# Kernel tuning notes

Hardware: AMD Instinct MI355X
Metric: run time of the kernel (lower is better)

The kernel has to match this reference:

```python
import jax, jax.numpy as jnp
import numpy as np

EPS = 1e-6


def _min_max_norm(v):
    # torch: 2.0 + (v - v.min()) / (v.max() - v.min()), global scalars
    mn, mx = v.min(), v.max()
    return 2.0 + (v - mn) / (mx - mn)


def setup_inputs() -> dict:
    key = jax.random.key(0)
    k1, k2, k3 = jax.random.split(key, 3)
    B, C, H, W = 2, 32, 96, 128
    return {
        "queries": jax.random.normal(k1, (B, C, H, W), jnp.float32),
        "keys": jax.random.normal(k2, (B, C, H, W), jnp.float32),
        "values": jax.random.normal(k3, (B, C, H, W), jnp.float32),
    }


def reference(queries, keys, values):
    B, C, H, W = queries.shape

    def row_column_softmax(s):  # s: [B,C,H,W]
        rc = jax.nn.softmax(s, axis=3) + jax.nn.softmax(s, axis=2)
        return rc / rc.max()

    def per_channel(q_c):  # q_c: [B,H,W] -> one output channel
        q = jnp.broadcast_to(q_c[:, None], (B, C, H, W))  # repeat over C
        # q_k_transpose: [B,C,H,H] (einsum sums w and y independently)
        hxh = jnp.einsum('bchw,bcxy->bchx', q, keys) + EPS
        # q_transpose_k: [B,C,W,W]
        wxw = jnp.einsum('bchw,bcxy->bcwy', q, keys) + EPS
        h_row = _min_max_norm(hxh.sum(axis=2))  # [B,C,H]  ('bcij->bcj')
        h_col = _min_max_norm(hxh.sum(axis=3))  # [B,C,H]  ('bcij->bci')
        w_row = _min_max_norm(wxw.sum(axis=2))  # [B,C,W]
        w_col = _min_max_norm(wxw.sum(axis=3))  # [B,C,W]
        outer = lambda m, n: jnp.einsum('bch,bcw->bchw', m, n)
        score = (row_column_softmax(outer(h_row, w_row))
                 + row_column_softmax(outer(h_row, w_col))
                 + row_column_softmax(outer(h_col, w_row))
                 + row_column_softmax(outer(h_col, w_col)))
        score = score / score.max()
        z_c = jnp.einsum('bchw,bchw->bhw', score, values)  # [B,H,W]
        return z_c, score

    # vectorize the original Python loop over query channels
    z_all, scores = jax.vmap(per_channel)(jnp.moveaxis(queries, 1, 0))
    z = jnp.swapaxes(z_all, 0, 1)  # [B,C,H,W]
    # torch returns the atten_score of the LAST loop iteration
    return z, scores[-1]
```

## Files before the change

kernel.cpp:

```cpp
#include <hip/hip_runtime.h>
#include <float.h>

#define BB 2
#define CC 32
#define HH 96
#define WW 128
#define HW (HH*WW)
#define BC (BB*CC)
#define NPLANE (BC*HW)
#define EPSF 1e-6f
#define LOG2E 1.4426950408889634f

#define QR_OFF 0
#define QC_OFF (QR_OFF + BC*HH)
#define QS_OFF (QC_OFF + BC*WW)
#define KR_OFF (QS_OFF + BC)
#define KC_OFF (KR_OFF + BC*HH)
#define KS_OFF (KC_OFF + BC*WW)
#define REC_OFF (KS_OFF + BC)
#define RECSZ 1344
#define BMX_OFF (REC_OFF + CC*BC*RECSZ)
#define BSX_OFF (BMX_OFF + CC*BC*4)

__device__ __forceinline__ float rcpf(float x) { return __builtin_amdgcn_rcpf(x); }
__device__ __forceinline__ float e2(float x) { return __builtin_amdgcn_exp2f(x); }

__device__ __forceinline__ float blkmax4(float v) {
  __shared__ float sred[4];
  #pragma unroll
  for (int o = 32; o > 0; o >>= 1) v = fmaxf(v, __shfl_xor(v, o, 64));
  if ((threadIdx.x & 63) == 0) sred[threadIdx.x >> 6] = v;
  __syncthreads();
  float r = fmaxf(fmaxf(sred[0], sred[1]), fmaxf(sred[2], sred[3]));
  __syncthreads();
  return r;
}

__global__ __launch_bounds__(256) void k1_plane_sums(const float* __restrict__ q,
                                                     const float* __restrict__ k,
                                                     float* __restrict__ ws) {
  int pb = blockIdx.x;
  int plane = pb & (BC - 1);
  const float* src = (pb < BC ? q : k) + (size_t)plane * HW;
  float* rowO = ws + (pb < BC ? QR_OFF : KR_OFF) + plane * HH;
  float* colO = ws + (pb < BC ? QC_OFF : KC_OFF) + plane * WW;
  float* totO = ws + (pb < BC ? QS_OFF : KS_OFF) + plane;
  __shared__ float cp[4 * WW];
  __shared__ float rsh[HH];
  __shared__ float wtot[2];
  int tid = threadIdx.x;
  int u = tid >> 6, l = tid & 63;
  float csum0 = 0.f, csum1 = 0.f;
  #pragma unroll 4
  for (int r = 0; r < 24; ++r) {
    int h = u * 24 + r;
    float v0 = src[h * WW + l];
    float v1 = src[h * WW + l + 64];
    csum0 += v0; csum1 += v1;
    float rs = v0 + v1;
    #pragma unroll
    for (int o = 1; o < 64; o <<= 1) rs += __shfl_xor(rs, o, 64);
    if (l == 0) { rowO[h] = rs; rsh[h] = rs; }
  }
  cp[u * WW + l] = csum0;
  cp[u * WW + l + 64] = csum1;
  __syncthreads();
  if (tid < WW) colO[tid] = cp[tid] + cp[WW + tid] + cp[2 * WW + tid] + cp[3 * WW + tid];
  float tv = (tid < HH) ? rsh[tid] : 0.f;
  if (tid < 128) {
    #pragma unroll
    for (int o = 1; o < 64; o <<= 1) tv += __shfl_xor(tv, o, 64);
    if ((tid & 63) == 0) wtot[tid >> 6] = tv;
  }
  __syncthreads();
  if (tid == 0) *totO = wtot[0] + wtot[1];
}

__device__ __forceinline__ float k2_raw(const float* __restrict__ ws, int type, int c0, int i, int L) {
  int bc = i / L, x = i - bc * L;
  int b = bc >> 5;
  if (type == 0) return ws[QS_OFF + b * CC + c0] * ws[KR_OFF + bc * HH + x] + HH * EPSF;
  if (type == 1) return ws[QR_OFF + (b * CC + c0) * HH + x] * ws[KS_OFF + bc] + HH * EPSF;
  if (type == 2) return ws[QS_OFF + b * CC + c0] * ws[KC_OFF + bc * WW + x] + WW * EPSF;
  return ws[QC_OFF + (b * CC + c0) * WW + x] * ws[KS_OFF + bc] + WW * EPSF;
}

__global__ __launch_bounds__(256) void k2_vec_norm(float* __restrict__ ws) {
  int c0 = blockIdx.x >> 2, type = blockIdx.x & 3;
  int L = (type < 2) ? HH : WW;
  int N = BC * L;
  int tid = threadIdx.x;
  float mx = -FLT_MAX, mn = FLT_MAX;
  for (int i = tid; i < N; i += 256) {
    float v = k2_raw(ws, type, c0, i, L);
    mx = fmaxf(mx, v); mn = fminf(mn, v);
  }
  mx = blkmax4(mx);
  mn = -blkmax4(-mn);
  float scale = rcpf(mx - mn);
  float fold = (type < 2) ? LOG2E : 1.0f;
  int fieldbase = (type == 0) ? 0 : (type == 1) ? 96 : (type == 2) ? 192 : 320;
  for (int i = tid; i < N; i += 256) {
    int bc = i / L, x = i - bc * L;
    float v = k2_raw(ws, type, c0, i, L);
    ws[REC_OFF + (size_t)(c0 * BC + bc) * RECSZ + fieldbase + x] =
        (2.0f + (v - mn) * scale) * fold;
  }
}

__global__ __launch_bounds__(128) void k3_rc(float* __restrict__ ws) {
  int g = blockIdx.x;
  int vb = g >> 1, pair = g & 1;
  float* rec = ws + REC_OFF + (size_t)vb * RECSZ;
  int tid = threadIdx.x;
  int u = tid >> 6, l = tid & 63;
  int t = pair * 2 + u;
  __shared__ __align__(16) float mn[448];
  __shared__ float rCl[2][WW];
  for (int i = tid; i < 112; i += 128) ((float4*)mn)[i] = ((const float4*)rec)[i];
  __syncthreads();
  const float* mv = mn + pair * 96;
  const float* nv = mn + 192 + u * 128;
  float n0 = nv[l], n1 = nv[l + 64];
  float cs0 = 0.f, cs1 = 0.f;
  #pragma unroll 6
  for (int h = 0; h < HH; h += 4) {
    float4 mp = *(const float4*)&mv[h];
    cs0 += e2(mp.x * n0) + e2(mp.y * n0) + e2(mp.z * n0) + e2(mp.w * n0);
    cs1 += e2(mp.x * n1) + e2(mp.y * n1) + e2(mp.z * n1) + e2(mp.w * n1);
  }
  float rc0 = rcpf(cs0), rc1 = rcpf(cs1);
  rCl[u][l] = rc0; rCl[u][l + 64] = rc1;
  rec[832 + 4 * l + t] = rc0;
  rec[832 + 4 * (l + 64) + t] = rc1;
  int h0 = l >> 1, hf = l & 1;
  float m0 = mv[h0], m1 = mv[h0 + 32], m2 = mv[h0 + 64];
  const float* nb = nv + 64 * hf;
  float s0 = 0.f, s1 = 0.f, s2 = 0.f;
  #pragma unroll 4
  for (int j = 0; j < 64; j += 4) {
    float4 np = *(const float4*)&nb[j];
    s0 += e2(m0 * np.x) + e2(m0 * np.y) + e2(m0 * np.z) + e2(m0 * np.w);
    s1 += e2(m1 * np.x) + e2(m1 * np.y) + e2(m1 * np.z) + e2(m1 * np.w);
    s2 += e2(m2 * np.x) + e2(m2 * np.y) + e2(m2 * np.z) + e2(m2 * np.w);
  }
  s0 += __shfl_xor(s0, 1, 64);
  s1 += __shfl_xor(s1, 1, 64);
  s2 += __shfl_xor(s2, 1, 64);
  float rr0 = rcpf(s0), rr1 = rcpf(s1), rr2 = rcpf(s2);
  if (hf == 0) {
    rec[448 + 4 * h0 + t] = rr0;
    rec[448 + 4 * (h0 + 32) + t] = rr1;
    rec[448 + 4 * (h0 + 64) + t] = rr2;
  }
  __syncthreads();
  const float* rcb = &rCl[u][64 * hf];
  float mx = 0.f;
  #pragma unroll 4
  for (int j = 0; j < 64; j += 4) {
    float4 np = *(const float4*)&nb[j];
    float4 rc = *(const float4*)&rcb[j];
    mx = fmaxf(mx, fmaxf(e2(m0 * np.x) * (rr0 + rc.x), e2(m0 * np.y) * (rr0 + rc.y)));
    mx = fmaxf(mx, fmaxf(e2(m0 * np.z) * (rr0 + rc.z), e2(m0 * np.w) * (rr0 + rc.w)));
    mx = fmaxf(mx, fmaxf(e2(m1 * np.x) * (rr1 + rc.x), e2(m1 * np.y) * (rr1 + rc.y)));
    mx = fmaxf(mx, fmaxf(e2(m1 * np.z) * (rr1 + rc.z), e2(m1 * np.w) * (rr1 + rc.w)));
    mx = fmaxf(mx, fmaxf(e2(m2 * np.x) * (rr2 + rc.x), e2(m2 * np.y) * (rr2 + rc.y)));
    mx = fmaxf(mx, fmaxf(e2(m2 * np.z) * (rr2 + rc.z), e2(m2 * np.w) * (rr2 + rc.w)));
  }
  #pragma unroll
  for (int o = 1; o < 64; o <<= 1) mx = fmaxf(mx, __shfl_xor(mx, o, 64));
  if (l == 0) ws[BMX_OFF + vb * 4 + t] = mx;
}

#define ELEMS 2
#define TILES 24
#define GRP 4
__global__ __launch_bounds__(256) void k4_score(const float* __restrict__ values,
                                                float* __restrict__ ws,
                                                float* __restrict__ out) {
  int bx = blockIdx.x;
  int tile = bx % TILES;
  int cb = bx / TILES;
  int b = cb & 1, c0 = cb >> 1;
  int tid = threadIdx.x;
  int base = tile * 512;
  int w = tid & 127;
  __shared__ __align__(16) float nS[GRP][256];
  __shared__ __align__(16) float c4S[GRP][512];
  __shared__ __align__(16) float mrf[CC * 24];
  __shared__ float s44[4][4];
  const float* rec0 = ws + REC_OFF + (size_t)(c0 * BC + b * CC) * RECSZ;
  float bm = ws[BMX_OFF + c0 * 256 + tid];
  #pragma unroll
  for (int o = 4; o <= 32; o <<= 1) bm = fmaxf(bm, __shfl_xor(bm, o, 64));
  if ((tid & 63) < 4) s44[tid >> 6][tid & 3] = bm;
  if (tid < 192) {
    int ch = tid / 6, f = tid - 6 * (tid / 6);
    const float* rsrc = rec0 + (size_t)ch * RECSZ;
    int soff = (f == 0) ? tile * 4 : (f == 1) ? 96 + tile * 4 : 448 + 16 * tile + 4 * (f - 2);
    *(float4*)&mrf[ch * 24 + f * 4] = *(const float4*)(rsrc + soff);
  }
  #pragma unroll
  for (int i = tid; i < GRP * 192; i += 256) {
    int chl = i / 192, rem = i - 192 * (i / 192);
    const float* rsrc = rec0 + (size_t)chl * RECSZ;
    float4 g4 = (rem < 64) ? *(const float4*)(rsrc + 192 + 4 * rem)
                           : *(const float4*)(rsrc + 832 + 4 * (rem - 64));
    if (rem < 64) *(float4*)&nS[chl][4 * rem] = g4;
    else          *(float4*)&c4S[chl][4 * (rem - 64)] = g4;
  }
  const float* vsrc0 = values + (size_t)(b * CC) * HW + base + tid;
  float v0 = vsrc0[0], v1 = vsrc0[256];
  __syncthreads();
  float im0 = rcpf(fmaxf(fmaxf(s44[0][0], s44[1][0]), fmaxf(s44[2][0], s44[3][0])));
  float im1 = rcpf(fmaxf(fmaxf(s44[0][1], s44[1][1]), fmaxf(s44[2][1], s44[3][1])));
  float im2 = rcpf(fmaxf(fmaxf(s44[0][2], s44[1][2]), fmaxf(s44[2][2], s44[3][2])));
  float im3 = rcpf(fmaxf(fmaxf(s44[0][3], s44[1][3]), fmaxf(s44[2][3], s44[3][3])));
  int r0 = tid >> 7;
  float U0 = 0.f, U1 = 0.f, smaxl = 0.f;
  for (int c = 0; c < CC; ++c) {
    if ((c & (GRP - 1)) == 0 && c) {
      __syncthreads();
      #pragma unroll
      for (int i = tid; i < GRP * 192; i += 256) {
        int chl = i / 192, rem = i - 192 * (i / 192);
        const float* rsrc = rec0 + (size_t)(c + chl) * RECSZ;
        float4 g4 = (rem < 64) ? *(const float4*)(rsrc + 192 + 4 * rem)
                               : *(const float4*)(rsrc + 832 + 4 * (rem - 64));
        if (rem < 64) *(float4*)&nS[chl][4 * rem] = g4;
        else          *(float4*)&c4S[chl][4 * (rem - 64)] = g4;
      }
      __syncthreads();
    }
    float nv0 = 0.f, nv1 = 0.f;
    if (c + 1 < CC) {
      nv0 = vsrc0[(size_t)(c + 1) * HW];
      nv1 = vsrc0[(size_t)(c + 1) * HW + 256];
    }
    int cl = c & (GRP - 1);
    float nr = nS[cl][w], nc = nS[cl][128 + w];
    float4 c4 = *(const float4*)&c4S[cl][4 * w];
    float A0 = c4.x * im0, A1 = c4.y * im1, A2 = c4.z * im2, A3 = c4.w * im3;
    const float* mc = &mrf[c * 24];
    #pragma unroll
    for (int j = 0; j < ELEMS; ++j) {
      int r = r0 + 2 * j;
      float mR = mc[r], mC = mc[4 + r];
      float4 r4 = *(const float4*)&mc[8 + 4 * r];
      float gx = fmaf(r4.x, im0, A0);
      float gy = fmaf(r4.y, im1, A1);
      float gz = fmaf(r4.z, im2, A2);
      float gw = fmaf(r4.w, im3, A3);
      float sc = e2(mR * nr) * gx + e2(mR * nc) * gy
               + e2(mC * nr) * gz + e2(mC * nc) * gw;
      smaxl = fmaxf(smaxl, sc);
      float uv = sc * (j == 0 ? v0 : v1);
      if (j == 0) U0 += uv; else U1 += uv;
    }
    v0 = nv0; v1 = nv1;
  }
  float* zout = out + (size_t)(b * CC + c0) * HW + base + tid;
  zout[0] = U0;
  zout[256] = U1;
  smaxl = blkmax4(smaxl);
  if (tid == 0) ws[BSX_OFF + bx] = smaxl;
}

#define K5_ZB (BC * 8)
__global__ __launch_bounds__(256) void k5_final(float* __restrict__ out,
                                                const float* __restrict__ ws) {
  int bx = blockIdx.x;
  int tid = threadIdx.x;
  if (bx < K5_ZB) {
    int p = bx >> 3, sub = bx & 7;
    int c0 = p & (CC - 1);
    __shared__ float sm;
    if (tid < 64) {
      float a = (tid < 48) ? ws[BSX_OFF + c0 * 48 + tid] : 0.f;
      #pragma unroll
      for (int o = 1; o < 64; o <<= 1) a = fmaxf(a, __shfl_xor(a, o, 64));
      if (tid == 0) sm = a;
    }
    __syncthreads();
    float ism = rcpf(sm);
    int off = p * HW + sub * 1536 + tid;
    #pragma unroll
    for (int j = 0; j < 6; ++j) out[off + 256 * j] *= ism;
  } else {
    int sp = bx - K5_ZB;
    int plane = sp >> 1, half = sp & 1;
    const float* rec = ws + REC_OFF + (size_t)((CC - 1) * BC + plane) * RECSZ;
    __shared__ __align__(16) float R[RECSZ];
    __shared__ float s44[4][4];
    __shared__ float sm;
    for (int i = tid; i < RECSZ / 4; i += 256) ((float4*)R)[i] = ((const float4*)rec)[i];
    float bm = ws[BMX_OFF + (CC - 1) * 256 + tid];
    #pragma unroll
    for (int o = 4; o <= 32; o <<= 1) bm = fmaxf(bm, __shfl_xor(bm, o, 64));
    if ((tid & 63) < 4) s44[tid >> 6][tid & 3] = bm;
    if (tid < 64) {
      float a = (tid < 48) ? ws[BSX_OFF + (CC - 1) * 48 + tid] : 0.f;
      #pragma unroll
      for (int o = 1; o < 64; o <<= 1) a = fmaxf(a, __shfl_xor(a, o, 64));
      if (tid == 0) sm = a;
    }
    __syncthreads();
    float im0 = rcpf(fmaxf(fmaxf(s44[0][0], s44[1][0]), fmaxf(s44[2][0], s44[3][0])));
    float im1 = rcpf(fmaxf(fmaxf(s44[0][1], s44[1][1]), fmaxf(s44[2][1], s44[3][1])));
    float im2 = rcpf(fmaxf(fmaxf(s44[0][2], s44[1][2]), fmaxf(s44[2][2], s44[3][2])));
    float im3 = rcpf(fmaxf(fmaxf(s44[0][3], s44[1][3]), fmaxf(s44[2][3], s44[3][3])));
    float isml = rcpf(sm);
    float* sout = out + (size_t)NPLANE + (size_t)plane * HW + half * 6144;
    #pragma unroll 4
    for (int e = tid; e < 6144; e += 256) {
      int idx = half * 6144 + e;
      int h = idx >> 7, ww = idx & 127;
      float mR = R[h], mC = R[96 + h];
      float nr = R[192 + ww], nc = R[320 + ww];
      float4 r4 = *(const float4*)&R[448 + 4 * h];
      float4 c4 = *(const float4*)&R[832 + 4 * ww];
      float A0 = c4.x * im0, A1 = c4.y * im1, A2 = c4.z * im2, A3 = c4.w * im3;
      float sc = e2(mR * nr) * fmaf(r4.x, im0, A0) + e2(mR * nc) * fmaf(r4.y, im1, A1)
               + e2(mC * nr) * fmaf(r4.z, im2, A2) + e2(mC * nc) * fmaf(r4.w, im3, A3);
      sout[e] = sc * isml;
    }
  }
}

extern "C" void kernel_launch(void* const* d_in, const int* in_sizes, int n_in,
                              void* d_out, int out_size, void* d_ws, size_t ws_size,
                              hipStream_t stream) {
  const float* q = (const float*)d_in[0];
  const float* k = (const float*)d_in[1];
  const float* v = (const float*)d_in[2];
  float* out = (float*)d_out;
  float* ws = (float*)d_ws;
  k1_plane_sums<<<2 * BC, 256, 0, stream>>>(q, k, ws);
  k2_vec_norm<<<CC * 4, 256, 0, stream>>>(ws);
  k3_rc<<<CC * BC * 2, 128, 0, stream>>>(ws);
  k4_score<<<CC * BB * TILES, 256, 0, stream>>>(v, ws, out);
  k5_final<<<K5_ZB + 128, 256, 0, stream>>>(out, ws);
}
```

Before: 114.2 us.

## Cache exponentials as fp16 in LDS for k3 and prefold max reciprocals in k4

k3 now computes each exp2 only once per (h,w) pair. It stores the results as packed fp16 in shared memory and reuses them for the row sums, via fdot2, and for the max pass, via packed f16 mul/add/max. Work moves to one block per softmax term with 256 threads. In k4 the inverse block maxima are folded into the staged row and column reciprocals, so the inner loop drops four FMAs per element. The fp16 path with 4096 scaling risks precision loss or overflow in the max estimate.

```diff
diff --git a/kernel.cpp b/kernel.cpp
--- a/kernel.cpp
+++ b/kernel.cpp
@@ -24,6 +24,36 @@
 
 __device__ __forceinline__ float rcpf(float x) { return __builtin_amdgcn_rcpf(x); }
 __device__ __forceinline__ float e2(float x) { return __builtin_amdgcn_exp2f(x); }
+
+typedef _Float16 h2v __attribute__((ext_vector_type(2)));
+__device__ __forceinline__ unsigned pkrtz_u(float a, float b) {
+  return __builtin_bit_cast(unsigned, __builtin_amdgcn_cvt_pkrtz(a, b));
+}
+__device__ __forceinline__ unsigned pk_add(unsigned a, unsigned b) {
+  unsigned d; asm("v_pk_add_f16 %0, %1, %2" : "=v"(d) : "v"(a), "v"(b)); return d;
+}
+__device__ __forceinline__ unsigned pk_mul(unsigned a, unsigned b) {
+  unsigned d; asm("v_pk_mul_f16 %0, %1, %2" : "=v"(d) : "v"(a), "v"(b)); return d;
+}
+__device__ __forceinline__ unsigned pk_max(unsigned a, unsigned b) {
+  unsigned d; asm("v_pk_max_f16 %0, %1, %2" : "=v"(d) : "v"(a), "v"(b)); return d;
+}
+__device__ __forceinline__ float dot2acc(unsigned u, float acc) {
+#if __has_builtin(__builtin_amdgcn_fdot2)
+  h2v a = __builtin_bit_cast(h2v, u);
+  h2v one = {(_Float16)1.0f, (_Float16)1.0f};
+  return __builtin_amdgcn_fdot2(a, one, acc, false);
+#else
+  float lo = (float)__builtin_bit_cast(_Float16, (unsigned short)(u & 0xffff));
+  float hi = (float)__builtin_bit_cast(_Float16, (unsigned short)(u >> 16));
+  return acc + lo + hi;
+#endif
+}
+__device__ __forceinline__ float h2max_f(unsigned u) {
+  float lo = (float)__builtin_bit_cast(_Float16, (unsigned short)(u & 0xffff));
+  float hi = (float)__builtin_bit_cast(_Float16, (unsigned short)(u >> 16));
+  return fmaxf(lo, hi);
+}
 
 __device__ __forceinline__ float blkmax4(float v) {
   __shared__ float sred[4];
@@ -108,68 +138,78 @@
   }
 }
 
-__global__ __launch_bounds__(128) void k3_rc(float* __restrict__ ws) {
+#define EPH 136
+__global__ __launch_bounds__(256) void k3_rc(float* __restrict__ ws) {
   int g = blockIdx.x;
-  int vb = g >> 1, pair = g & 1;
+  int vb = g >> 2, t = g & 3;
   float* rec = ws + REC_OFF + (size_t)vb * RECSZ;
   int tid = threadIdx.x;
   int u = tid >> 6, l = tid & 63;
-  int t = pair * 2 + u;
-  __shared__ __align__(16) float mn[448];
-  __shared__ float rCl[2][WW];
-  for (int i = tid; i < 112; i += 128) ((float4*)mn)[i] = ((const float4*)rec)[i];
-  __syncthreads();
-  const float* mv = mn + pair * 96;
-  const float* nv = mn + 192 + u * 128;
-  float n0 = nv[l], n1 = nv[l + 64];
+  __shared__ __align__(16) unsigned short eh[HH * EPH];
+  __shared__ __align__(16) float mncp[512];
+  __shared__ __align__(16) unsigned short rch[128];
+  __shared__ float wmx[3];
+  const float* mv = rec + (t >> 1) * 96;
+  const float* nv = rec + 192 + (t & 1) * 128;
+  if (tid < 224) mncp[tid] = (tid < 96) ? mv[tid] : nv[tid - 96];
+  __syncthreads();
+  float n0 = mncp[96 + 2 * l], n1 = mncp[96 + 2 * l + 1];
   float cs0 = 0.f, cs1 = 0.f;
   #pragma unroll 6
-  for (int h = 0; h < HH; h += 4) {
-    float4 mp = *(const float4*)&mv[h];
-    cs0 += e2(mp.x * n0) + e2(mp.y * n0) + e2(mp.z * n0) + e2(mp.w * n0);
-    cs1 += e2(mp.x * n1) + e2(mp.y * n1) + e2(mp.z * n1) + e2(mp.w * n1);
-  }
-  float rc0 = rcpf(cs0), rc1 = rcpf(cs1);
-  rCl[u][l] = rc0; rCl[u][l + 64] = rc1;
-  rec[832 + 4 * l + t] = rc0;
-  rec[832 + 4 * (l + 64) + t] = rc1;
-  int h0 = l >> 1, hf = l & 1;
-  float m0 = mv[h0], m1 = mv[h0 + 32], m2 = mv[h0 + 64];
-  const float* nb = nv + 64 * hf;
-  float s0 = 0.f, s1 = 0.f, s2 = 0.f;
-  #pragma unroll 4
-  for (int j = 0; j < 64; j += 4) {
-    float4 np = *(const float4*)&nb[j];
-    s0 += e2(m0 * np.x) + e2(m0 * np.y) + e2(m0 * np.z) + e2(m0 * np.w);
-    s1 += e2(m1 * np.x) + e2(m1 * np.y) + e2(m1 * np.z) + e2(m1 * np.w);
-    s2 += e2(m2 * np.x) + e2(m2 * np.y) + e2(m2 * np.z) + e2(m2 * np.w);
-  }
-  s0 += __shfl_xor(s0, 1, 64);
-  s1 += __shfl_xor(s1, 1, 64);
-  s2 += __shfl_xor(s2, 1, 64);
-  float rr0 = rcpf(s0), rr1 = rcpf(s1), rr2 = rcpf(s2);
-  if (hf == 0) {
-    rec[448 + 4 * h0 + t] = rr0;
-    rec[448 + 4 * (h0 + 32) + t] = rr1;
-    rec[448 + 4 * (h0 + 64) + t] = rr2;
-  }
-  __syncthreads();
-  const float* rcb = &rCl[u][64 * hf];
+  for (int r = 0; r < 24; ++r) {
+    int h = u * 24 + r;
+    float m = mncp[h];
+    float e0 = e2(m * n0);
+    float e1 = e2(m * n1);
+    cs0 += e0; cs1 += e1;
+    *(unsigned*)&eh[h * EPH + 2 * l] = pkrtz_u(e0, e1);
+  }
+  __syncthreads();
+  mncp[u * 128 + 2 * l] = cs0;
+  mncp[u * 128 + 2 * l + 1] = cs1;
+  __syncthreads();
+  if (tid < 64) {
+    int w0 = 2 * tid, w1 = w0 + 1;
+    float rc0 = rcpf(mncp[w0] + mncp[128 + w0] + mncp[256 + w0] + mncp[384 + w0]);
+    float rc1 = rcpf(mncp[w1] + mncp[128 + w1] + mncp[256 + w1] + mncp[384 + w1]);
+    rec[832 + 4 * w0 + t] = rc0;
+    rec[832 + 4 * w1 + t] = rc1;
+    ((unsigned*)rch)[tid] = pkrtz_u(rc0 * 4096.f, rc1 * 4096.f);
+  }
+  __syncthreads();
   float mx = 0.f;
-  #pragma unroll 4
-  for (int j = 0; j < 64; j += 4) {
-    float4 np = *(const float4*)&nb[j];
-    float4 rc = *(const float4*)&rcb[j];
-    mx = fmaxf(mx, fmaxf(e2(m0 * np.x) * (rr0 + rc.x), e2(m0 * np.y) * (rr0 + rc.y)));
-    mx = fmaxf(mx, fmaxf(e2(m0 * np.z) * (rr0 + rc.z), e2(m0 * np.w) * (rr0 + rc.w)));
-    mx = fmaxf(mx, fmaxf(e2(m1 * np.x) * (rr1 + rc.x), e2(m1 * np.y) * (rr1 + rc.y)));
-    mx = fmaxf(mx, fmaxf(e2(m1 * np.z) * (rr1 + rc.z), e2(m1 * np.w) * (rr1 + rc.w)));
-    mx = fmaxf(mx, fmaxf(e2(m2 * np.x) * (rr2 + rc.x), e2(m2 * np.y) * (rr2 + rc.y)));
-    mx = fmaxf(mx, fmaxf(e2(m2 * np.z) * (rr2 + rc.z), e2(m2 * np.w) * (rr2 + rc.w)));
-  }
-  #pragma unroll
-  for (int o = 1; o < 64; o <<= 1) mx = fmaxf(mx, __shfl_xor(mx, o, 64));
-  if (l == 0) ws[BMX_OFF + vb * 4 + t] = mx;
+  if (tid < 192) {
+    int row = tid >> 1, hf = tid & 1;
+    const uint4* ep = (const uint4*)&eh[row * EPH + hf * 64];
+    float s = 0.f;
+    #pragma unroll
+    for (int j = 0; j < 8; ++j) {
+      uint4 ev = ep[j];
+      s = dot2acc(ev.x, s); s = dot2acc(ev.y, s);
+      s = dot2acc(ev.z, s); s = dot2acc(ev.w, s);
+    }
+    s += __shfl_xor(s, 1, 64);
+    float rr = rcpf(s);
+    if (hf == 0) rec[448 + 4 * row + t] = rr;
+    unsigned rr2 = pkrtz_u(rr * 4096.f, rr * 4096.f);
+    unsigned mxu = 0;
+    const uint4* cp2 = (const uint4*)&rch[hf * 64];
+    #pragma unroll
+    for (int j = 0; j < 8; ++j) {
+      uint4 ev = ep[j];
+      uint4 cv = cp2[j];
+      mxu = pk_max(mxu, pk_mul(ev.x, pk_add(cv.x, rr2)));
+      mxu = pk_max(mxu, pk_mul(ev.y, pk_add(cv.y, rr2)));
+      mxu = pk_max(mxu, pk_mul(ev.z, pk_add(cv.z, rr2)));
+      mxu = pk_max(mxu, pk_mul(ev.w, pk_add(cv.w, rr2)));
+    }
+    mx = h2max_f(mxu) * (1.0f / 4096.f);
+    #pragma unroll
+    for (int o = 1; o < 64; o <<= 1) mx = fmaxf(mx, __shfl_xor(mx, o, 64));
+    if ((tid & 63) == 0) wmx[tid >> 6] = mx;
+  }
+  __syncthreads();
+  if (tid == 0) ws[BMX_OFF + vb * 4 + t] = fmaxf(fmaxf(wmx[0], wmx[1]), wmx[2]);
 }
 
 #define ELEMS 2
@@ -200,22 +240,31 @@
     int soff = (f == 0) ? tile * 4 : (f == 1) ? 96 + tile * 4 : 448 + 16 * tile + 4 * (f - 2);
     *(float4*)&mrf[ch * 24 + f * 4] = *(const float4*)(rsrc + soff);
   }
+  const float* vsrc0 = values + (size_t)(b * CC) * HW + base + tid;
+  float v0 = vsrc0[0], v1 = vsrc0[256];
+  __syncthreads();
+  float im0 = rcpf(fmaxf(fmaxf(s44[0][0], s44[1][0]), fmaxf(s44[2][0], s44[3][0])));
+  float im1 = rcpf(fmaxf(fmaxf(s44[0][1], s44[1][1]), fmaxf(s44[2][1], s44[3][1])));
+  float im2 = rcpf(fmaxf(fmaxf(s44[0][2], s44[1][2]), fmaxf(s44[2][2], s44[3][2])));
+  float im3 = rcpf(fmaxf(fmaxf(s44[0][3], s44[1][3]), fmaxf(s44[2][3], s44[3][3])));
+  for (int i = tid; i < CC * 16; i += 256) {
+    int ch = i >> 4, kk = i & 15, tt = kk & 3;
+    float sel = tt == 0 ? im0 : tt == 1 ? im1 : tt == 2 ? im2 : im3;
+    mrf[ch * 24 + 8 + kk] *= sel;
+  }
   #pragma unroll
   for (int i = tid; i < GRP * 192; i += 256) {
     int chl = i / 192, rem = i - 192 * (i / 192);
     const float* rsrc = rec0 + (size_t)chl * RECSZ;
-    float4 g4 = (rem < 64) ? *(const float4*)(rsrc + 192 + 4 * rem)
-                           : *(const float4*)(rsrc + 832 + 4 * (rem - 64));
-    if (rem < 64) *(float4*)&nS[chl][4 * rem] = g4;
-    else          *(float4*)&c4S[chl][4 * (rem - 64)] = g4;
-  }
-  const float* vsrc0 = values + (size_t)(b * CC) * HW + base + tid;
-  float v0 = vsrc0[0], v1 = vsrc0[256];
-  __syncthreads();
-  float im0 = rcpf(fmaxf(fmaxf(s44[0][0], s44[1][0]), fmaxf(s44[2][0], s44[3][0])));
-  float im1 = rcpf(fmaxf(fmaxf(s44[0][1], s44[1][1]), fmaxf(s44[2][1], s44[3][1])));
-  float im2 = rcpf(fmaxf(fmaxf(s44[0][2], s44[1][2]), fmaxf(s44[2][2], s44[3][2])));
-  float im3 = rcpf(fmaxf(fmaxf(s44[0][3], s44[1][3]), fmaxf(s44[2][3], s44[3][3])));
+    if (rem < 64) {
+      *(float4*)&nS[chl][4 * rem] = *(const float4*)(rsrc + 192 + 4 * rem);
+    } else {
+      float4 g4 = *(const float4*)(rsrc + 832 + 4 * (rem - 64));
+      g4.x *= im0; g4.y *= im1; g4.z *= im2; g4.w *= im3;
+      *(float4*)&c4S[chl][4 * (rem - 64)] = g4;
+    }
+  }
+  __syncthreads();
   int r0 = tid >> 7;
   float U0 = 0.f, U1 = 0.f, smaxl = 0.f;
   for (int c = 0; c < CC; ++c) {
@@ -225,10 +274,13 @@
       for (int i = tid; i < GRP * 192; i += 256) {
         int chl = i / 192, rem = i - 192 * (i / 192);
         const float* rsrc = rec0 + (size_t)(c + chl) * RECSZ;
-        float4 g4 = (rem < 64) ? *(const float4*)(rsrc + 192 + 4 * rem)
-                               : *(const float4*)(rsrc + 832 + 4 * (rem - 64));
-        if (rem < 64) *(float4*)&nS[chl][4 * rem] = g4;
-        else          *(float4*)&c4S[chl][4 * (rem - 64)] = g4;
+        if (rem < 64) {
+          *(float4*)&nS[chl][4 * rem] = *(const float4*)(rsrc + 192 + 4 * rem);
+        } else {
+          float4 g4 = *(const float4*)(rsrc + 832 + 4 * (rem - 64));
+          g4.x *= im0; g4.y *= im1; g4.z *= im2; g4.w *= im3;
+          *(float4*)&c4S[chl][4 * (rem - 64)] = g4;
+        }
       }
       __syncthreads();
     }
@@ -240,19 +292,14 @@
     int cl = c & (GRP - 1);
     float nr = nS[cl][w], nc = nS[cl][128 + w];
     float4 c4 = *(const float4*)&c4S[cl][4 * w];
-    float A0 = c4.x * im0, A1 = c4.y * im1, A2 = c4.z * im2, A3 = c4.w * im3;
     const float* mc = &mrf[c * 24];
     #pragma unroll
     for (int j = 0; j < ELEMS; ++j) {
       int r = r0 + 2 * j;
       float mR = mc[r], mC = mc[4 + r];
       float4 r4 = *(const float4*)&mc[8 + 4 * r];
-      float gx = fmaf(r4.x, im0, A0);
-      float gy = fmaf(r4.y, im1, A1);
-      float gz = fmaf(r4.z, im2, A2);
-      float gw = fmaf(r4.w, im3, A3);
-      float sc = e2(mR * nr) * gx + e2(mR * nc) * gy
-               + e2(mC * nr) * gz + e2(mC * nc) * gw;
+      float sc = e2(mR * nr) * (r4.x + c4.x) + e2(mR * nc) * (r4.y + c4.y)
+               + e2(mC * nr) * (r4.z + c4.z) + e2(mC * nc) * (r4.w + c4.w);
       smaxl = fmaxf(smaxl, sc);
       float uv = sc * (j == 0 ? v0 : v1);
       if (j == 0) U0 += uv; else U1 += uv;
@@ -337,7 +384,7 @@
   float* ws = (float*)d_ws;
   k1_plane_sums<<<2 * BC, 256, 0, stream>>>(q, k, ws);
   k2_vec_norm<<<CC * 4, 256, 0, stream>>>(ws);
-  k3_rc<<<CC * BC * 2, 128, 0, stream>>>(ws);
+  k3_rc<<<CC * BC * 4, 256, 0, stream>>>(ws);
   k4_score<<<CC * BB * TILES, 256, 0, stream>>>(v, ws, out);
   k5_final<<<K5_ZB + 128, 256, 0, stream>>>(out, ws);
 }
```

New measurement: 99.83 us. 1.14x faster.
